# Performance work log

Measured on AMD Instinct MI355X. Metric: run time of the kernel, lower is better.

The kernel has to match this reference:

```python
import math
import jax, jax.numpy as jnp
import numpy as np
from jax import lax

MUL = 16           # multiplicity of 0e and 1o in input and output irreps
NRB = 8            # num_radial_basis
DIAMETER = 3.0
STEPS = (1.0, 1.0, 1.0)
DIM = 4 * MUL      # 16 scalars + 16 vectors * 3 = 64 channels


def _constants():
    # lattice from __init__: arange(-s, s+1) * step per axis, s = floor(r/step)
    r = DIAMETER / 2
    axes = [np.arange(-math.floor(r / st), math.floor(r / st) + 1.0) * st for st in STEPS]
    lattice = np.stack(np.meshgrid(*axes, indexing='ij'), axis=-1)  # [Kx,Ky,Kz,3]
    d = np.linalg.norm(lattice, axis=-1)                            # [Kx,Ky,Kz]
    # soft_one_hot_linspace(basis='smooth_finite', cutoff=True)
    values = np.linspace(0.0, r, NRB + 2)[1:-1]
    step = values[1] - values[0]
    diff = (d[..., None] - values) / step
    inside = diff ** 2 < 1.0
    emb = np.where(inside, 1.14136 * np.exp(2.0) * np.exp(-2.0 / np.where(inside, 1.0 - diff ** 2, 1.0)), 0.0)
    # spherical harmonics, normalize=True, normalization='component'
    n = lattice / np.maximum(d[..., None], 1e-12)  # unit vectors; 0 at the origin voxel
    sh0 = np.ones_like(d)                          # Y_0 (component normalized)
    sh1 = np.sqrt(3.0) * n                         # Y_1 (component normalized)
    return emb.astype(np.float32), sh0.astype(np.float32), sh1.astype(np.float32)

EMB, SH0, SH1 = _constants()
KX, KY, KZ = SH0.shape  # 3,3,3


def setup_inputs() -> dict:
    key = jax.random.key(0)
    ks = jax.random.split(key, 7)
    B, G = 4, 32
    return {
        'x': jax.random.normal(ks[0], (B, G, G, G, DIM), jnp.float32),
        'W_sc0': jax.random.normal(ks[1], (MUL, MUL), jnp.float32),  # Linear 0e->0e
        'W_sc1': jax.random.normal(ks[2], (MUL, MUL), jnp.float32),  # Linear 1o->1o
        'w1': jax.random.normal(ks[3], (NRB, MUL, MUL), jnp.float32),  # path 0e x 0e -> 0e
        'w2': jax.random.normal(ks[4], (NRB, MUL, MUL), jnp.float32),  # path 0e x 1o -> 1o
        'w3': jax.random.normal(ks[5], (NRB, MUL, MUL), jnp.float32),  # path 1o x 0e -> 1o
        'w4': jax.random.normal(ks[6], (NRB, MUL, MUL), jnp.float32),  # path 1o x 1o -> 0e
    }


def _kernel(w1, w2, w3, w4):
    # radial basis -> per-voxel path weights, divided by kernel volume (as in source)
    emb, sh0, sh1 = jnp.asarray(EMB), jnp.asarray(SH0), jnp.asarray(SH1)
    norm = float(KX * KY * KZ)
    W1, W2, W3, W4 = [jnp.einsum('xyzk,kio->xyzio', emb, w) / norm for w in (w1, w2, w3, w4)]
    # path normalization: each output irrep receives 2 paths of fan_in mul*1 = 16 -> 1/sqrt(32)
    alpha = 1.0 / np.sqrt(2.0 * MUL)
    # tp.right blocks (Clebsch-Gordan contractions, lmax=1):
    k00 = alpha * W1 * sh0[..., None, None]                                              # [.,i,o]
    k01 = alpha * jnp.einsum('xyzio,xyzm->xyziom', W2, sh1).reshape(KX, KY, KZ, MUL, 3 * MUL)
    k10 = (alpha / np.sqrt(3.0)) * jnp.einsum('xyzio,xyzm->xyzimo', W4, sh1).reshape(KX, KY, KZ, 3 * MUL, MUL)
    k11 = alpha * jnp.einsum('xyzio,mn->xyzimon', W3 * sh0[..., None, None],
                             jnp.eye(3, dtype=W3.dtype)).reshape(KX, KY, KZ, 3 * MUL, 3 * MUL)
    return jnp.concatenate([jnp.concatenate([k00, k01], axis=-1),
                            jnp.concatenate([k10, k11], axis=-1)], axis=-2)  # [Kx,Ky,Kz,64,64]


def reference(x, W_sc0, W_sc1, w1, w2, w3, w4):
    B, X, Y, Z, _ = x.shape
    inv_sqrt_mul = 1.0 / np.sqrt(MUL)
    # self-connection: e3nn Linear per irrep (applied pointwise over b,x,y,z)
    xs = x[..., :MUL]                                   # [B,X,Y,Z,16] scalars
    xv = x[..., MUL:].reshape(B, X, Y, Z, MUL, 3)       # [B,X,Y,Z,16,3] vectors
    sc_s = (xs @ W_sc0) * inv_sqrt_mul
    sc_v = jnp.einsum('bxyzic,io->bxyzoc', xv, W_sc1) * inv_sqrt_mul
    sc = jnp.concatenate([sc_s, sc_v.reshape(B, X, Y, Z, 3 * MUL)], axis=-1)
    # position-dependent equivariant kernel + standard 3D conv
    k = _kernel(w1, w2, w3, w4)
    conv = lax.conv_general_dilated(x, k, (1, 1, 1), 'SAME',
                                    dimension_numbers=('NXYZC', 'XYZIO', 'NXYZC'))
    return sc + conv
```

## Files before the change

### kernel.cpp

```cpp
#include <hip/hip_runtime.h>

typedef unsigned short u16;
typedef unsigned int u32;
typedef __bf16 bf16x8 __attribute__((ext_vector_type(8)));
typedef float f32x4 __attribute__((ext_vector_type(4)));
typedef u32 u32x4 __attribute__((ext_vector_type(4)));

__device__ __align__(16) u16 g_kTr[27 * 8 * 512];

__device__ __forceinline__ u16 f2bf(float f) {
    unsigned int u = __float_as_uint(f);
    u += 0x7FFFu + ((u >> 16) & 1u);
    return (u16)(u >> 16);
}

__device__ __forceinline__ u32 pack_bf(float a, float b) {
    u32 ua = __float_as_uint(a) + 0x8000u;
    u32 ub = __float_as_uint(b) + 0x8000u;
    return __builtin_amdgcn_perm(ub, ua, 0x07060302u);
}

__global__ __launch_bounds__(64) void build_k(
    const float* __restrict__ Wsc0, const float* __restrict__ Wsc1,
    const float* __restrict__ w1, const float* __restrict__ w2,
    const float* __restrict__ w3, const float* __restrict__ w4)
{
    const int t = blockIdx.x;
    const int c = threadIdx.x;
    const int dx = t / 9 - 1, dy = (t / 3) % 3 - 1, dz = t % 3 - 1;
    const float d = sqrtf((float)(dx * dx + dy * dy + dz * dz));
    const float step = 1.5f / 9.0f;
    float emb[8];
#pragma unroll
    for (int k = 0; k < 8; ++k) {
        float diff = (d - (float)(k + 1) * step) / step;
        float q = diff * diff;
        emb[k] = (q < 1.0f) ? 1.14136f * expf(2.0f - 2.0f / (1.0f - q)) : 0.0f;
    }
    const float dn = fmaxf(d, 1e-12f);
    const float s3 = 1.7320508075688772f;
    const float sh1[3] = { s3 * dx / dn, s3 * dy / dn, s3 * dz / dn };
    const float alpha  = 0.17677669529663687f;
    const float alpha3 = alpha * 0.57735026918962576f;

    const int base2 = ((t * 2 + (c >> 5)) * 2 + ((c >> 4) & 1)) * 2;
    const int l15c  = c & 15;
    auto put = [&](int r, float v) {
        g_kTr[(base2 + (r >> 5)) * 512 + (((r >> 3) & 3) * 16 + l15c) * 8 + (r & 7)] =
            f2bf(v);
    };

    if (c < 16) {
        const int o = c;
#pragma unroll
        for (int i = 0; i < 16; ++i) {
            float W1 = 0.f, W4 = 0.f;
#pragma unroll
            for (int k = 0; k < 8; ++k) {
                W1 += emb[k] * w1[k * 256 + i * 16 + o];
                W4 += emb[k] * w4[k * 256 + i * 16 + o];
            }
            W1 *= (1.0f / 27.0f); W4 *= (1.0f / 27.0f);
            float v0 = alpha * W1;
            if (t == 13) v0 += 0.25f * Wsc0[i * 16 + o];
            put(i, v0);
            const float base = alpha3 * W4;
#pragma unroll
            for (int m = 0; m < 3; ++m) put(16 + 3 * i + m, base * sh1[m]);
        }
    } else {
        const int o = (c - 16) / 3, nc = (c - 16) % 3;
#pragma unroll
        for (int i = 0; i < 16; ++i) {
            float W2 = 0.f, W3 = 0.f;
#pragma unroll
            for (int k = 0; k < 8; ++k) {
                W2 += emb[k] * w2[k * 256 + i * 16 + o];
                W3 += emb[k] * w3[k * 256 + i * 16 + o];
            }
            W2 *= (1.0f / 27.0f); W3 *= (1.0f / 27.0f);
            put(i, alpha * W2 * sh1[nc]);
#pragma unroll
            for (int m = 0; m < 3; ++m) {
                float v = (m == nc) ? alpha * W3 : 0.0f;
                if (t == 13 && m == nc) v += 0.25f * Wsc1[i * 16 + o];
                put(16 + 3 * i + m, v);
            }
        }
    }
}

#define LDSW7 24576

#define ISSUE_B(s, t) \
  { const char* _p = bTr + (t) * 8192; \
    asm volatile("global_load_dwordx4 %0, %4, off\n\t" \
                 "global_load_dwordx4 %1, %4, off offset:1024\n\t" \
                 "global_load_dwordx4 %2, %4, off offset:2048\n\t" \
                 "global_load_dwordx4 %3, %4, off offset:3072" \
                 : "=&v"(B##s##0), "=&v"(B##s##1), "=&v"(B##s##2), "=&v"(B##s##3) \
                 : "v"(_p)); }

#define LOADA2(s, i0, i1, RCC) { \
  const int _r  = rbase + (RCC); \
  const int _o0 = _r * 128 + ((kg ^ (_r & 7)) << 4); \
  A##s##_##i0 = *reinterpret_cast<const bf16x8*>(abase + _o0); \
  A##s##_##i1 = *reinterpret_cast<const bf16x8*>(abase + (_o0 ^ 64)); }

#define RCC7(T, YY) (((T)/9)*128 + ((((T)/3)%3) + (YY))*18 + ((T)%3))

#define LOAD_A4(s, T) \
  LOADA2(s, 0, 1, RCC7(T,0)) \
  LOADA2(s, 2, 3, RCC7(T,1))

#define WAITV(N) \
  asm volatile("s_waitcnt vmcnt(" #N ")" ::: "memory"); \
  __builtin_amdgcn_sched_barrier(0);

#define BC(x) __builtin_bit_cast(bf16x8, x)
#define MF(b_, a_, c_) __builtin_amdgcn_mfma_f32_16x16x32_bf16(BC(b_), a_, c_, 0, 0, 0)

#define MFMA8(bs, as) \
  acc00 = MF(B##bs##0, A##as##_0, acc00); acc01 = MF(B##bs##2, A##as##_0, acc01); \
  acc10 = MF(B##bs##0, A##as##_2, acc10); acc11 = MF(B##bs##2, A##as##_2, acc11); \
  acc00 = MF(B##bs##1, A##as##_1, acc00); acc01 = MF(B##bs##3, A##as##_1, acc01); \
  acc10 = MF(B##bs##1, A##as##_3, acc10); acc11 = MF(B##bs##3, A##as##_3, acc11);

__global__ __launch_bounds__(256, 3) void conv_mfma8(
    const float* __restrict__ x, float* __restrict__ out)
{
    __shared__ __align__(16) u16 xt[LDSW7];

    const int bid0 = blockIdx.x;
    const int bid  = (bid0 & 7) * 256 + (bid0 >> 3);
    const int b    = bid >> 9;
    const int X    = (bid >> 4) & 31;
    const int yg   = (bid >> 1) & 7;
    const int zg   = bid & 1;
    const int y0   = yg << 2;
    const int z0   = zg << 4;
    const int tid  = threadIdx.x;
    const int wv   = tid >> 6;
    const int lane = tid & 63;
    const int l15  = lane & 15;
    const int kg   = lane >> 4;
    const int yh   = wv >> 1;
    const int nh   = wv & 1;

    const char* bTr = (const char*)g_kTr + nh * 4096 + lane * 16;

    u32x4 B00, B01, B02, B03, B10, B11, B12, B13, B20, B21, B22, B23;
    bf16x8 A0_0, A0_1, A0_2, A0_3;
    bf16x8 A1_0, A1_1, A1_2, A1_3;

    ISSUE_B(0, 1)
    ISSUE_B(1, 3)

    {
        const int rloc = lane >> 3;
        const int swz  = (lane & 7) ^ rloc;
        const int cip  = wv * 4;
        const int rip0 = cip * 8 + rloc;
#pragma unroll 1
        for (int p = 0; p < 3; ++p) {
            const int xin = X + p - 1;
#pragma unroll
            for (int j = 0; j < 4; ++j) {
                const int rip = rip0 + j * 8;
                const int yi  = rip / 18;
                const int zid = rip - yi * 18;
                const int yin = y0 + yi - 1;
                const int zin = z0 + zid - 1;
                const bool inb = (rip < 108) & ((unsigned)xin < 32u)
                               & ((unsigned)yin < 32u) & ((unsigned)zin < 32u);
                u32x4 pk = {0u, 0u, 0u, 0u};
                if (inb) {
                    const float4* s = reinterpret_cast<const float4*>(
                        x + ((size_t)(((b * 32 + xin) * 32 + yin) * 32 + zin) * 64
                             + swz * 8));
                    float4 v0 = s[0], v1 = s[1];
                    pk[0] = pack_bf(v0.x, v0.y); pk[1] = pack_bf(v0.z, v0.w);
                    pk[2] = pack_bf(v1.x, v1.y); pk[3] = pack_bf(v1.z, v1.w);
                }
                *reinterpret_cast<u32x4*>(&xt[(p * 16 + cip + j) * 512 + lane * 8]) = pk;
            }
        }
    }
    __syncthreads();

    const char* abase = reinterpret_cast<const char*>(xt);
    const int rbase = yh * 36 + l15;

    const f32x4 z4 = {0.f, 0.f, 0.f, 0.f};
    f32x4 acc00 = z4, acc01 = z4, acc10 = z4, acc11 = z4;

    LOAD_A4(0, 1)
    ISSUE_B(2, 4)   LOAD_A4(1, 3)            MFMA8(0, 0)
    ISSUE_B(0, 5)   LOAD_A4(0, 4)            MFMA8(1, 1)
    ISSUE_B(1, 7)   LOAD_A4(1, 5)  WAITV(8)  MFMA8(2, 0)
    ISSUE_B(2, 9)   LOAD_A4(0, 7)  WAITV(8)  MFMA8(0, 1)
    ISSUE_B(0, 10)  LOAD_A4(1, 9)  WAITV(8)  MFMA8(1, 0)
    ISSUE_B(1, 11)  LOAD_A4(0, 10) WAITV(8)  MFMA8(2, 1)
    ISSUE_B(2, 12)  LOAD_A4(1, 11) WAITV(8)  MFMA8(0, 0)
    ISSUE_B(0, 13)  LOAD_A4(0, 12) WAITV(8)  MFMA8(1, 1)
    ISSUE_B(1, 14)  LOAD_A4(1, 13) WAITV(8)  MFMA8(2, 0)
    ISSUE_B(2, 15)  LOAD_A4(0, 14) WAITV(8)  MFMA8(0, 1)
    ISSUE_B(0, 16)  LOAD_A4(1, 15) WAITV(8)  MFMA8(1, 0)
    ISSUE_B(1, 17)  LOAD_A4(0, 16) WAITV(8)  MFMA8(2, 1)
    ISSUE_B(2, 19)  LOAD_A4(1, 17) WAITV(8)  MFMA8(0, 0)
    ISSUE_B(0, 21)  LOAD_A4(0, 19) WAITV(8)  MFMA8(1, 1)
    ISSUE_B(1, 22)  LOAD_A4(1, 21) WAITV(8)  MFMA8(2, 0)
    ISSUE_B(2, 23)  LOAD_A4(0, 22) WAITV(8)  MFMA8(0, 1)
    ISSUE_B(0, 25)  LOAD_A4(1, 23) WAITV(8)  MFMA8(1, 0)
                    LOAD_A4(0, 25) WAITV(4)  MFMA8(2, 1)
                                   WAITV(0)  MFMA8(0, 0)

    float* obase = out + ((((size_t)(b * 32 + X) * 32 + (y0 + yh * 2)) * 32) + z0) * 64
                 + nh * 32 + kg * 4;
    *reinterpret_cast<f32x4*>(obase + l15 * 64)               = acc00;
    *reinterpret_cast<f32x4*>(obase + l15 * 64 + 16)          = acc01;
    *reinterpret_cast<f32x4*>(obase + 2048 + l15 * 64)        = acc10;
    *reinterpret_cast<f32x4*>(obase + 2048 + l15 * 64 + 16)   = acc11;
}

extern "C" void kernel_launch(void* const* d_in, const int* in_sizes, int n_in,
                              void* d_out, int out_size, void* d_ws, size_t ws_size,
                              hipStream_t stream)
{
    const float* x    = (const float*)d_in[0];
    const float* Wsc0 = (const float*)d_in[1];
    const float* Wsc1 = (const float*)d_in[2];
    const float* w1   = (const float*)d_in[3];
    const float* w2   = (const float*)d_in[4];
    const float* w3   = (const float*)d_in[5];
    const float* w4   = (const float*)d_in[6];
    float* out = (float*)d_out;

    build_k<<<dim3(27), dim3(64), 0, stream>>>(Wsc0, Wsc1, w1, w2, w3, w4);
    conv_mfma8<<<dim3(2048), dim3(256), 0, stream>>>(x, out);
}
```

Before: 57.12 us.

## Pre-convert input to bf16 and use persistent double-buffered async-LDS conv kernel

Adds a prep pass that converts x to bf16 into workspace, merged into the same launch as the kernel-weight build. The new conv kernel runs 256 large-LDS blocks, each handling 4 tiles of 4 y-rows, with an 8-accumulator MFMA tile. It streams the next tile's halo into a second LDS buffer with global_load_lds while computing the current tile. This targets the fp32 conversion and load latency in the old conv, but costs an extra full pass over x and runs at low occupancy with a rigid hand-tuned wait schedule.

```diff
diff --git a/kernel.cpp b/kernel.cpp
--- a/kernel.cpp
+++ b/kernel.cpp
@@ -6,13 +6,10 @@
 typedef float f32x4 __attribute__((ext_vector_type(4)));
 typedef u32 u32x4 __attribute__((ext_vector_type(4)));
 
+#define AS1 __attribute__((address_space(1)))
+#define AS3 __attribute__((address_space(3)))
+
 __device__ __align__(16) u16 g_kTr[27 * 8 * 512];
-
-__device__ __forceinline__ u16 f2bf(float f) {
-    unsigned int u = __float_as_uint(f);
-    u += 0x7FFFu + ((u >> 16) & 1u);
-    return (u16)(u >> 16);
-}
 
 __device__ __forceinline__ u32 pack_bf(float a, float b) {
     u32 ua = __float_as_uint(a) + 0x8000u;
@@ -20,77 +17,95 @@
     return __builtin_amdgcn_perm(ub, ua, 0x07060302u);
 }
 
-__global__ __launch_bounds__(64) void build_k(
+__global__ __launch_bounds__(256) void prep(
     const float* __restrict__ Wsc0, const float* __restrict__ Wsc1,
     const float* __restrict__ w1, const float* __restrict__ w2,
-    const float* __restrict__ w3, const float* __restrict__ w4)
+    const float* __restrict__ w3, const float* __restrict__ w4,
+    const float* __restrict__ x, u16* __restrict__ xb, u32* __restrict__ zp)
 {
-    const int t = blockIdx.x;
-    const int c = threadIdx.x;
-    const int dx = t / 9 - 1, dy = (t / 3) % 3 - 1, dz = t % 3 - 1;
-    const float d = sqrtf((float)(dx * dx + dy * dy + dz * dz));
-    const float step = 1.5f / 9.0f;
-    float emb[8];
-#pragma unroll
-    for (int k = 0; k < 8; ++k) {
-        float diff = (d - (float)(k + 1) * step) / step;
-        float q = diff * diff;
-        emb[k] = (q < 1.0f) ? 1.14136f * expf(2.0f - 2.0f / (1.0f - q)) : 0.0f;
-    }
-    const float dn = fmaxf(d, 1e-12f);
-    const float s3 = 1.7320508075688772f;
-    const float sh1[3] = { s3 * dx / dn, s3 * dy / dn, s3 * dz / dn };
-    const float alpha  = 0.17677669529663687f;
-    const float alpha3 = alpha * 0.57735026918962576f;
-
-    const int base2 = ((t * 2 + (c >> 5)) * 2 + ((c >> 4) & 1)) * 2;
-    const int l15c  = c & 15;
-    auto put = [&](int r, float v) {
-        g_kTr[(base2 + (r >> 5)) * 512 + (((r >> 3) & 3) * 16 + l15c) * 8 + (r & 7)] =
-            f2bf(v);
-    };
-
-    if (c < 16) {
-        const int o = c;
-#pragma unroll
-        for (int i = 0; i < 16; ++i) {
-            float W1 = 0.f, W4 = 0.f;
-#pragma unroll
-            for (int k = 0; k < 8; ++k) {
-                W1 += emb[k] * w1[k * 256 + i * 16 + o];
-                W4 += emb[k] * w4[k * 256 + i * 16 + o];
+    const int tid = threadIdx.x;
+    if (blockIdx.x < 27) {
+        if (tid >= 64) return;
+        const int t = blockIdx.x;
+        const int c = tid;
+        const int dx = t / 9 - 1, dy = (t / 3) % 3 - 1, dz = t % 3 - 1;
+        const float d = sqrtf((float)(dx * dx + dy * dy + dz * dz));
+        const float step = 1.5f / 9.0f;
+        float emb[8];
+#pragma unroll
+        for (int k = 0; k < 8; ++k) {
+            float diff = (d - (float)(k + 1) * step) / step;
+            float q = diff * diff;
+            emb[k] = (q < 1.0f) ? 1.14136f * expf(2.0f - 2.0f / (1.0f - q)) : 0.0f;
+        }
+        const float dn = fmaxf(d, 1e-12f);
+        const float s3 = 1.7320508075688772f;
+        const float sh1[3] = { s3 * dx / dn, s3 * dy / dn, s3 * dz / dn };
+        const float alpha  = 0.17677669529663687f;
+        const float alpha3 = alpha * 0.57735026918962576f;
+
+        const int base2 = ((t * 2 + (c >> 5)) * 2 + ((c >> 4) & 1)) * 2;
+        const int l15c  = c & 15;
+        auto put = [&](int r, float v) {
+            u32 u = __float_as_uint(v);
+            u += 0x7FFFu + ((u >> 16) & 1u);
+            g_kTr[(base2 + (r >> 5)) * 512 + (((r >> 3) & 3) * 16 + l15c) * 8 + (r & 7)] =
+                (u16)(u >> 16);
+        };
+
+        if (c < 16) {
+            const int o = c;
+#pragma unroll
+            for (int i = 0; i < 16; ++i) {
+                float W1 = 0.f, W4 = 0.f;
+#pragma unroll
+                for (int k = 0; k < 8; ++k) {
+                    W1 += emb[k] * w1[k * 256 + i * 16 + o];
+                    W4 += emb[k] * w4[k * 256 + i * 16 + o];
+                }
+                W1 *= (1.0f / 27.0f); W4 *= (1.0f / 27.0f);
+                float v0 = alpha * W1;
+                if (t == 13) v0 += 0.25f * Wsc0[i * 16 + o];
+                put(i, v0);
+                const float base = alpha3 * W4;
+#pragma unroll
+                for (int m = 0; m < 3; ++m) put(16 + 3 * i + m, base * sh1[m]);
             }
-            W1 *= (1.0f / 27.0f); W4 *= (1.0f / 27.0f);
-            float v0 = alpha * W1;
-            if (t == 13) v0 += 0.25f * Wsc0[i * 16 + o];
-            put(i, v0);
-            const float base = alpha3 * W4;
-#pragma unroll
-            for (int m = 0; m < 3; ++m) put(16 + 3 * i + m, base * sh1[m]);
+        } else {
+            const int o = (c - 16) / 3, nc = (c - 16) % 3;
+#pragma unroll
+            for (int i = 0; i < 16; ++i) {
+                float W2 = 0.f, W3 = 0.f;
+#pragma unroll
+                for (int k = 0; k < 8; ++k) {
+                    W2 += emb[k] * w2[k * 256 + i * 16 + o];
+                    W3 += emb[k] * w3[k * 256 + i * 16 + o];
+                }
+                W2 *= (1.0f / 27.0f); W3 *= (1.0f / 27.0f);
+                put(i, alpha * W2 * sh1[nc]);
+#pragma unroll
+                for (int m = 0; m < 3; ++m) {
+                    float v = (m == nc) ? alpha * W3 : 0.0f;
+                    if (t == 13 && m == nc) v += 0.25f * Wsc1[i * 16 + o];
+                    put(16 + 3 * i + m, v);
+                }
+            }
         }
     } else {
-        const int o = (c - 16) / 3, nc = (c - 16) % 3;
-#pragma unroll
-        for (int i = 0; i < 16; ++i) {
-            float W2 = 0.f, W3 = 0.f;
-#pragma unroll
-            for (int k = 0; k < 8; ++k) {
-                W2 += emb[k] * w2[k * 256 + i * 16 + o];
-                W3 += emb[k] * w3[k * 256 + i * 16 + o];
-            }
-            W2 *= (1.0f / 27.0f); W3 *= (1.0f / 27.0f);
-            put(i, alpha * W2 * sh1[nc]);
-#pragma unroll
-            for (int m = 0; m < 3; ++m) {
-                float v = (m == nc) ? alpha * W3 : 0.0f;
-                if (t == 13 && m == nc) v += 0.25f * Wsc1[i * 16 + o];
-                put(16 + 3 * i + m, v);
-            }
+        const int bid2 = blockIdx.x - 27;
+        if (bid2 == 0) {
+            u32x4 z = {0u, 0u, 0u, 0u};
+            *reinterpret_cast<u32x4*>(zp + tid * 4) = z;
         }
+        const size_t base = ((size_t)bid2 * 256 + tid) * 8;
+        const float4* s = reinterpret_cast<const float4*>(x + base);
+        float4 v0 = s[0], v1 = s[1];
+        u32x4 p;
+        p[0] = pack_bf(v0.x, v0.y); p[1] = pack_bf(v0.z, v0.w);
+        p[2] = pack_bf(v1.x, v1.y); p[3] = pack_bf(v1.z, v1.w);
+        *reinterpret_cast<u32x4*>(xb + base) = p;
     }
 }
-
-#define LDSW7 24576
 
 #define ISSUE_B(s, t) \
   { const char* _p = bTr + (t) * 8192; \
@@ -107,18 +122,159 @@
   A##s##_##i0 = *reinterpret_cast<const bf16x8*>(abase + _o0); \
   A##s##_##i1 = *reinterpret_cast<const bf16x8*>(abase + (_o0 ^ 64)); }
 
+#define WAITV(N) \
+  asm volatile("s_waitcnt vmcnt(" #N ")" ::: "memory"); \
+  __builtin_amdgcn_sched_barrier(0);
+
+#define BARRIER() \
+  asm volatile("s_waitcnt lgkmcnt(0)\n\ts_barrier" ::: "memory"); \
+  __builtin_amdgcn_sched_barrier(0);
+
+#define BC(x) __builtin_bit_cast(bf16x8, x)
+#define MF(b_, a_, c_) __builtin_amdgcn_mfma_f32_16x16x32_bf16(BC(b_), a_, c_, 0, 0, 0)
+
+#define BUFU16 39424
+
+#define STG(s) { \
+  const int _c   = wv * 20 + (s); \
+  const int _row = _c * 8 + rloc; \
+  const int _rid = _row / 204; \
+  const int _rem = _row - _rid * 204; \
+  const int _yi  = _rem / 34; \
+  const int _zid = _rem - _yi * 34; \
+  const int _xin = Xs + _rid - 1; \
+  const int _yin = ys0 + _yi - 1; \
+  const int _zin = _zid - 1; \
+  const bool _ib = (_row < 612) && ((unsigned)_xin < 32u) \
+                 && ((unsigned)_yin < 32u) && ((unsigned)_zin < 32u); \
+  const u16* _src = _ib \
+      ? xb + ((size_t)(((bs * 32 + _xin) * 32 + _yin) * 32 + _zin) * 64 + swz * 8) \
+      : zp16; \
+  u16* _dst = (_c < 77) ? (bufn + _c * 512) : (xt + 78848); \
+  __builtin_amdgcn_global_load_lds((const AS1 u32*)_src, (AS3 u32*)_dst, 16, 0, 0); \
+  __builtin_amdgcn_sched_barrier(0); }
+
+#define RCC4(T, YY, MT) ((((T)/9)*6 + (YY) + (((T)/3)%3))*34 + ((T)%3) + (MT)*16)
+
+#define LOAD_A8(s, T) \
+  LOADA2(s, 0, 1, RCC4(T,0,0)) \
+  LOADA2(s, 2, 3, RCC4(T,0,1)) \
+  LOADA2(s, 4, 5, RCC4(T,1,0)) \
+  LOADA2(s, 6, 7, RCC4(T,1,1))
+
+#define MFMA16(bs, as) \
+  acc000 = MF(B##bs##0, A##as##_0, acc000); acc001 = MF(B##bs##2, A##as##_0, acc001); \
+  acc010 = MF(B##bs##0, A##as##_2, acc010); acc011 = MF(B##bs##2, A##as##_2, acc011); \
+  acc100 = MF(B##bs##0, A##as##_4, acc100); acc101 = MF(B##bs##2, A##as##_4, acc101); \
+  acc110 = MF(B##bs##0, A##as##_6, acc110); acc111 = MF(B##bs##2, A##as##_6, acc111); \
+  acc000 = MF(B##bs##1, A##as##_1, acc000); acc001 = MF(B##bs##3, A##as##_1, acc001); \
+  acc010 = MF(B##bs##1, A##as##_3, acc010); acc011 = MF(B##bs##3, A##as##_3, acc011); \
+  acc100 = MF(B##bs##1, A##as##_5, acc100); acc101 = MF(B##bs##3, A##as##_5, acc101); \
+  acc110 = MF(B##bs##1, A##as##_7, acc110); acc111 = MF(B##bs##3, A##as##_7, acc111);
+
+__global__ __launch_bounds__(256, 1) void conv_mfma10(
+    const u16* __restrict__ xb, const u16* __restrict__ zp16,
+    float* __restrict__ out)
+{
+    extern __shared__ u16 xt[];
+
+    const int blk   = blockIdx.x;
+    const int tbase = ((blk & 7) * 32 + (blk >> 3)) * 4;
+    const int tid   = threadIdx.x;
+    const int wv    = tid >> 6;
+    const int lane  = tid & 63;
+    const int l15   = lane & 15;
+    const int kg    = lane >> 4;
+    const int yh    = wv >> 1;
+    const int nh    = wv & 1;
+    const int rloc  = lane >> 3;
+    const int swz   = (lane & 7) ^ rloc;
+    const int rbase = yh * 68 + l15;
+
+    const char* bTr = (const char*)g_kTr + nh * 4096 + lane * 16;
+
+    u32x4 B00, B01, B02, B03, B10, B11, B12, B13,
+          B20, B21, B22, B23, B30, B31, B32, B33;
+    bf16x8 A0_0, A0_1, A0_2, A0_3, A0_4, A0_5, A0_6, A0_7;
+    bf16x8 A1_0, A1_1, A1_2, A1_3, A1_4, A1_5, A1_6, A1_7;
+
+    {
+        const int ts = tbase;
+        const int bs = ts >> 8, Xs = (ts >> 3) & 31, ys0 = (ts & 7) << 2;
+        u16* bufn = xt;
+        STG(0)  STG(1)  STG(2)  STG(3)  STG(4)
+        STG(5)  STG(6)  STG(7)  STG(8)  STG(9)
+        STG(10) STG(11) STG(12) STG(13) STG(14)
+        STG(15) STG(16) STG(17) STG(18) STG(19)
+        WAITV(0)
+    }
+    ISSUE_B(0, 1)
+    ISSUE_B(1, 3)
+    ISSUE_B(2, 4)
+    BARRIER()
+
+#pragma unroll 1
+    for (int k = 0; k < 4; ++k) {
+        const u16* bufk = xt + (k & 1) * BUFU16;
+        u16*       bufn = xt + ((k & 1) ^ 1) * BUFU16;
+        const char* abase = (const char*)bufk;
+
+        const int tk = tbase + k;
+        const int b  = tk >> 8, X = (tk >> 3) & 31, y0 = (tk & 7) << 2;
+        const int ts = tbase + (k < 3 ? k + 1 : 3);
+        const int bs = ts >> 8, Xs = (ts >> 3) & 31, ys0 = (ts & 7) << 2;
+
+        const f32x4 z4 = {0.f, 0.f, 0.f, 0.f};
+        f32x4 acc000 = z4, acc001 = z4, acc010 = z4, acc011 = z4;
+        f32x4 acc100 = z4, acc101 = z4, acc110 = z4, acc111 = z4;
+
+        LOAD_A8(0, 1)
+        STG(0)  STG(1)  ISSUE_B(3, 5)   LOAD_A8(1, 3)   WAITV(14)  MFMA16(0, 0)
+        STG(2)  STG(3)  ISSUE_B(0, 7)   LOAD_A8(0, 4)   WAITV(16)  MFMA16(1, 1)
+        STG(4)  STG(5)  ISSUE_B(1, 9)   LOAD_A8(1, 5)   WAITV(18)  MFMA16(2, 0)
+        STG(6)  STG(7)  ISSUE_B(2, 10)  LOAD_A8(0, 7)   WAITV(18)  MFMA16(3, 1)
+        STG(8)  STG(9)  ISSUE_B(3, 11)  LOAD_A8(1, 9)   WAITV(18)  MFMA16(0, 0)
+        STG(10) STG(11) ISSUE_B(0, 12)  LOAD_A8(0, 10)  WAITV(18)  MFMA16(1, 1)
+        STG(12) STG(13) ISSUE_B(1, 13)  LOAD_A8(1, 11)  WAITV(18)  MFMA16(2, 0)
+        STG(14) STG(15) ISSUE_B(2, 14)  LOAD_A8(0, 12)  WAITV(18)  MFMA16(3, 1)
+        STG(16) STG(17) ISSUE_B(3, 15)  LOAD_A8(1, 13)  WAITV(18)  MFMA16(0, 0)
+        STG(18) STG(19) ISSUE_B(0, 16)  LOAD_A8(0, 14)  WAITV(18)  MFMA16(1, 1)
+                        ISSUE_B(1, 17)  LOAD_A8(1, 15)  WAITV(16)  MFMA16(2, 0)
+                        ISSUE_B(2, 19)  LOAD_A8(0, 16)  WAITV(14)  MFMA16(3, 1)
+                        ISSUE_B(3, 21)  LOAD_A8(1, 17)  WAITV(12)  MFMA16(0, 0)
+                        ISSUE_B(0, 22)  LOAD_A8(0, 19)  WAITV(12)  MFMA16(1, 1)
+                        ISSUE_B(1, 23)  LOAD_A8(1, 21)  WAITV(12)  MFMA16(2, 0)
+                        ISSUE_B(2, 25)  LOAD_A8(0, 22)  WAITV(12)  MFMA16(3, 1)
+                                        LOAD_A8(1, 23)  WAITV(8)   MFMA16(0, 0)
+                                        LOAD_A8(0, 25)  WAITV(4)   MFMA16(1, 1)
+                                                        WAITV(0)   MFMA16(2, 0)
+
+        float* obase = out + (((size_t)(b * 32 + X) * 32 + (y0 + yh * 2)) * 32) * 64
+                     + nh * 32 + kg * 4;
+        *reinterpret_cast<f32x4*>(obase + l15 * 64)                    = acc000;
+        *reinterpret_cast<f32x4*>(obase + l15 * 64 + 16)               = acc001;
+        *reinterpret_cast<f32x4*>(obase + (16 + l15) * 64)             = acc010;
+        *reinterpret_cast<f32x4*>(obase + (16 + l15) * 64 + 16)        = acc011;
+        *reinterpret_cast<f32x4*>(obase + 2048 + l15 * 64)             = acc100;
+        *reinterpret_cast<f32x4*>(obase + 2048 + l15 * 64 + 16)        = acc101;
+        *reinterpret_cast<f32x4*>(obase + 2048 + (16 + l15) * 64)      = acc110;
+        *reinterpret_cast<f32x4*>(obase + 2048 + (16 + l15) * 64 + 16) = acc111;
+        __builtin_amdgcn_sched_barrier(0);
+
+        ISSUE_B(0, 1)
+        ISSUE_B(1, 3)
+        ISSUE_B(2, 4)
+        BARRIER()
+    }
+}
+
+#define LDSW7 24576
+
 #define RCC7(T, YY) (((T)/9)*128 + ((((T)/3)%3) + (YY))*18 + ((T)%3))
 
 #define LOAD_A4(s, T) \
   LOADA2(s, 0, 1, RCC7(T,0)) \
   LOADA2(s, 2, 3, RCC7(T,1))
-
-#define WAITV(N) \
-  asm volatile("s_waitcnt vmcnt(" #N ")" ::: "memory"); \
-  __builtin_amdgcn_sched_barrier(0);
-
-#define BC(x) __builtin_bit_cast(bf16x8, x)
-#define MF(b_, a_, c_) __builtin_amdgcn_mfma_f32_16x16x32_bf16(BC(b_), a_, c_, 0, 0, 0)
 
 #define MFMA8(bs, as) \
   acc00 = MF(B##bs##0, A##as##_0, acc00); acc01 = MF(B##bs##2, A##as##_0, acc01); \
@@ -236,6 +392,16 @@
     const float* w4   = (const float*)d_in[6];
     float* out = (float*)d_out;
 
-    build_k<<<dim3(27), dim3(64), 0, stream>>>(Wsc0, Wsc1, w1, w2, w3, w4);
-    conv_mfma8<<<dim3(2048), dim3(256), 0, stream>>>(x, out);
+    const size_t xb_bytes = (size_t)4 * 32 * 32 * 32 * 64 * 2;
+    if (ws_size >= 4096 + xb_bytes) {
+        u32* zp = (u32*)d_ws;
+        u16* xb = (u16*)((char*)d_ws + 4096);
+        prep<<<dim3(27 + 4096), dim3(256), 0, stream>>>(Wsc0, Wsc1, w1, w2, w3, w4,
+                                                        x, xb, zp);
+        conv_mfma10<<<dim3(256), dim3(256), 158720, stream>>>(xb, (const u16*)zp, out);
+    } else {
+        prep<<<dim3(27), dim3(256), 0, stream>>>(Wsc0, Wsc1, w1, w2, w3, w4,
+                                                 x, (u16*)nullptr, (u32*)nullptr);
+        conv_mfma8<<<dim3(2048), dim3(256), 0, stream>>>(x, out);
+    }
 }
```

Measured after the change: 55.19 us. 1.03x faster.

## Use persistent blocks with double-buffered LDS staging of next tile

Applied to the files above, without the earlier changes.

Replaces the 2048-block conv kernel with 256 persistent blocks that each process four consecutive full-Z tiles of 4 y-rows. The halo for the next tile is loaded from global memory and packed into a second LDS buffer while MFMAs run on the current one, which hides staging latency behind compute. Each wave now owns twice as many output rows (8 accumulators), and B loads switch from inline asm with explicit vmcnt waits to plain loads ordered by sched barriers. The cost is roughly 154KB of dynamic LDS and one block per CU, so occupancy-based latency hiding is gone and the kernel depends on the compiler scheduling the interleaved loads well.

```diff
diff --git a/kernel.cpp b/kernel.cpp
--- a/kernel.cpp
+++ b/kernel.cpp
@@ -7,12 +7,6 @@
 typedef u32 u32x4 __attribute__((ext_vector_type(4)));
 
 __device__ __align__(16) u16 g_kTr[27 * 8 * 512];
-
-__device__ __forceinline__ u16 f2bf(float f) {
-    unsigned int u = __float_as_uint(f);
-    u += 0x7FFFu + ((u >> 16) & 1u);
-    return (u16)(u >> 16);
-}
 
 __device__ __forceinline__ u32 pack_bf(float a, float b) {
     u32 ua = __float_as_uint(a) + 0x8000u;
@@ -46,8 +40,10 @@
     const int base2 = ((t * 2 + (c >> 5)) * 2 + ((c >> 4) & 1)) * 2;
     const int l15c  = c & 15;
     auto put = [&](int r, float v) {
+        u32 u = __float_as_uint(v);
+        u += 0x7FFFu + ((u >> 16) & 1u);
         g_kTr[(base2 + (r >> 5)) * 512 + (((r >> 3) & 3) * 16 + l15c) * 8 + (r & 7)] =
-            f2bf(v);
+            (u16)(u >> 16);
     };
 
     if (c < 16) {
@@ -90,16 +86,13 @@
     }
 }
 
-#define LDSW7 24576
-
-#define ISSUE_B(s, t) \
-  { const char* _p = bTr + (t) * 8192; \
-    asm volatile("global_load_dwordx4 %0, %4, off\n\t" \
-                 "global_load_dwordx4 %1, %4, off offset:1024\n\t" \
-                 "global_load_dwordx4 %2, %4, off offset:2048\n\t" \
-                 "global_load_dwordx4 %3, %4, off offset:3072" \
-                 : "=&v"(B##s##0), "=&v"(B##s##1), "=&v"(B##s##2), "=&v"(B##s##3) \
-                 : "v"(_p)); }
+#define BUFU16 39424
+
+#define WALL() __builtin_amdgcn_sched_barrier(0);
+
+#define LOADB(S, T) { \
+  const u32x4* _p = reinterpret_cast<const u32x4*>(bTr + (T) * 8192); \
+  B##S##0 = _p[0]; B##S##1 = _p[64]; B##S##2 = _p[128]; B##S##3 = _p[192]; }
 
 #define LOADA2(s, i0, i1, RCC) { \
   const int _r  = rbase + (RCC); \
@@ -107,120 +100,145 @@
   A##s##_##i0 = *reinterpret_cast<const bf16x8*>(abase + _o0); \
   A##s##_##i1 = *reinterpret_cast<const bf16x8*>(abase + (_o0 ^ 64)); }
 
-#define RCC7(T, YY) (((T)/9)*128 + ((((T)/3)%3) + (YY))*18 + ((T)%3))
-
-#define LOAD_A4(s, T) \
-  LOADA2(s, 0, 1, RCC7(T,0)) \
-  LOADA2(s, 2, 3, RCC7(T,1))
-
-#define WAITV(N) \
-  asm volatile("s_waitcnt vmcnt(" #N ")" ::: "memory"); \
-  __builtin_amdgcn_sched_barrier(0);
+#define RCC4(T, YY, MT) ((((T)/9)*6 + (YY) + (((T)/3)%3))*34 + ((T)%3) + (MT)*16)
+
+#define LOAD_A8(s, T) \
+  LOADA2(s, 0, 1, RCC4(T,0,0)) \
+  LOADA2(s, 2, 3, RCC4(T,0,1)) \
+  LOADA2(s, 4, 5, RCC4(T,1,0)) \
+  LOADA2(s, 6, 7, RCC4(T,1,1))
+
+#define SLD(S, C) { \
+  const int _c   = wv * 20 + (C); \
+  const int _row = _c * 8 + rloc; \
+  const int _rid = _row / 204; \
+  const int _rem = _row - _rid * 204; \
+  const int _yi  = _rem / 34; \
+  const int _zid = _rem - _yi * 34; \
+  const int _xin = Xs + _rid - 1; \
+  const int _yin = ys0 + _yi - 1; \
+  const int _zin = _zid - 1; \
+  const bool _ib = (_row < 612) && ((unsigned)_xin < 32u) && \
+                   ((unsigned)_yin < 32u) && ((unsigned)_zin < 32u); \
+  F##S##a = (f32x4){0.f, 0.f, 0.f, 0.f}; \
+  F##S##b = (f32x4){0.f, 0.f, 0.f, 0.f}; \
+  if (_ib) { \
+    const f32x4* _p = reinterpret_cast<const f32x4*>( \
+        x + ((size_t)(((bs * 32 + _xin) * 32 + _yin) * 32 + _zin) * 64 + swz * 8)); \
+    F##S##a = _p[0]; F##S##b = _p[1]; \
+  } }
+
+#define SWR(S, C) { \
+  const int _c = wv * 20 + (C); \
+  if (_c < 77) { \
+    u32x4 _pk; \
+    _pk[0] = pack_bf(F##S##a[0], F##S##a[1]); \
+    _pk[1] = pack_bf(F##S##a[2], F##S##a[3]); \
+    _pk[2] = pack_bf(F##S##b[0], F##S##b[1]); \
+    _pk[3] = pack_bf(F##S##b[2], F##S##b[3]); \
+    *reinterpret_cast<u32x4*>(bufn + _c * 512 + lane * 8) = _pk; \
+  } }
 
 #define BC(x) __builtin_bit_cast(bf16x8, x)
 #define MF(b_, a_, c_) __builtin_amdgcn_mfma_f32_16x16x32_bf16(BC(b_), a_, c_, 0, 0, 0)
 
-#define MFMA8(bs, as) \
-  acc00 = MF(B##bs##0, A##as##_0, acc00); acc01 = MF(B##bs##2, A##as##_0, acc01); \
-  acc10 = MF(B##bs##0, A##as##_2, acc10); acc11 = MF(B##bs##2, A##as##_2, acc11); \
-  acc00 = MF(B##bs##1, A##as##_1, acc00); acc01 = MF(B##bs##3, A##as##_1, acc01); \
-  acc10 = MF(B##bs##1, A##as##_3, acc10); acc11 = MF(B##bs##3, A##as##_3, acc11);
-
-__global__ __launch_bounds__(256, 3) void conv_mfma8(
+#define MFMA16(bs, as) \
+  acc000 = MF(B##bs##0, A##as##_0, acc000); acc001 = MF(B##bs##2, A##as##_0, acc001); \
+  acc010 = MF(B##bs##0, A##as##_2, acc010); acc011 = MF(B##bs##2, A##as##_2, acc011); \
+  acc100 = MF(B##bs##0, A##as##_4, acc100); acc101 = MF(B##bs##2, A##as##_4, acc101); \
+  acc110 = MF(B##bs##0, A##as##_6, acc110); acc111 = MF(B##bs##2, A##as##_6, acc111); \
+  acc000 = MF(B##bs##1, A##as##_1, acc000); acc001 = MF(B##bs##3, A##as##_1, acc001); \
+  acc010 = MF(B##bs##1, A##as##_3, acc010); acc011 = MF(B##bs##3, A##as##_3, acc011); \
+  acc100 = MF(B##bs##1, A##as##_5, acc100); acc101 = MF(B##bs##3, A##as##_5, acc101); \
+  acc110 = MF(B##bs##1, A##as##_7, acc110); acc111 = MF(B##bs##3, A##as##_7, acc111);
+
+__global__ __launch_bounds__(256, 1) void conv_mfma11(
     const float* __restrict__ x, float* __restrict__ out)
 {
-    __shared__ __align__(16) u16 xt[LDSW7];
-
-    const int bid0 = blockIdx.x;
-    const int bid  = (bid0 & 7) * 256 + (bid0 >> 3);
-    const int b    = bid >> 9;
-    const int X    = (bid >> 4) & 31;
-    const int yg   = (bid >> 1) & 7;
-    const int zg   = bid & 1;
-    const int y0   = yg << 2;
-    const int z0   = zg << 4;
-    const int tid  = threadIdx.x;
-    const int wv   = tid >> 6;
-    const int lane = tid & 63;
-    const int l15  = lane & 15;
-    const int kg   = lane >> 4;
-    const int yh   = wv >> 1;
-    const int nh   = wv & 1;
+    extern __shared__ u16 xt[];
+
+    const int blk   = blockIdx.x;
+    const int tbase = ((blk & 7) * 32 + (blk >> 3)) * 4;
+    const int tid   = threadIdx.x;
+    const int wv    = tid >> 6;
+    const int lane  = tid & 63;
+    const int l15   = lane & 15;
+    const int kg    = lane >> 4;
+    const int yh    = wv >> 1;
+    const int nh    = wv & 1;
+    const int rloc  = lane >> 3;
+    const int swz   = (lane & 7) ^ rloc;
+    const int rbase = yh * 68 + l15;
 
     const char* bTr = (const char*)g_kTr + nh * 4096 + lane * 16;
 
     u32x4 B00, B01, B02, B03, B10, B11, B12, B13, B20, B21, B22, B23;
-    bf16x8 A0_0, A0_1, A0_2, A0_3;
-    bf16x8 A1_0, A1_1, A1_2, A1_3;
-
-    ISSUE_B(0, 1)
-    ISSUE_B(1, 3)
+    bf16x8 A0_0, A0_1, A0_2, A0_3, A0_4, A0_5, A0_6, A0_7;
+    bf16x8 A1_0, A1_1, A1_2, A1_3, A1_4, A1_5, A1_6, A1_7;
+    f32x4 F0a, F0b, F1a, F1b, F2a, F2b, F3a, F3b;
 
     {
-        const int rloc = lane >> 3;
-        const int swz  = (lane & 7) ^ rloc;
-        const int cip  = wv * 4;
-        const int rip0 = cip * 8 + rloc;
+        const int ts = tbase;
+        const int bs = ts >> 8, Xs = (ts >> 3) & 31, ys0 = (ts & 7) << 2;
+        u16* bufn = xt;
+#pragma unroll
+        for (int g = 0; g < 5; ++g) {
+            SLD(0, g * 4 + 0) SLD(1, g * 4 + 1) SLD(2, g * 4 + 2) SLD(3, g * 4 + 3)
+            SWR(0, g * 4 + 0) SWR(1, g * 4 + 1) SWR(2, g * 4 + 2) SWR(3, g * 4 + 3)
+        }
+    }
+    __syncthreads();
+
 #pragma unroll 1
-        for (int p = 0; p < 3; ++p) {
-            const int xin = X + p - 1;
-#pragma unroll
-            for (int j = 0; j < 4; ++j) {
-                const int rip = rip0 + j * 8;
-                const int yi  = rip / 18;
-                const int zid = rip - yi * 18;
-                const int yin = y0 + yi - 1;
-                const int zin = z0 + zid - 1;
-                const bool inb = (rip < 108) & ((unsigned)xin < 32u)
-                               & ((unsigned)yin < 32u) & ((unsigned)zin < 32u);
-                u32x4 pk = {0u, 0u, 0u, 0u};
-                if (inb) {
-                    const float4* s = reinterpret_cast<const float4*>(
-                        x + ((size_t)(((b * 32 + xin) * 32 + yin) * 32 + zin) * 64
-                             + swz * 8));
-                    float4 v0 = s[0], v1 = s[1];
-                    pk[0] = pack_bf(v0.x, v0.y); pk[1] = pack_bf(v0.z, v0.w);
-                    pk[2] = pack_bf(v1.x, v1.y); pk[3] = pack_bf(v1.z, v1.w);
-                }
-                *reinterpret_cast<u32x4*>(&xt[(p * 16 + cip + j) * 512 + lane * 8]) = pk;
-            }
-        }
-    }
-    __syncthreads();
-
-    const char* abase = reinterpret_cast<const char*>(xt);
-    const int rbase = yh * 36 + l15;
-
-    const f32x4 z4 = {0.f, 0.f, 0.f, 0.f};
-    f32x4 acc00 = z4, acc01 = z4, acc10 = z4, acc11 = z4;
-
-    LOAD_A4(0, 1)
-    ISSUE_B(2, 4)   LOAD_A4(1, 3)            MFMA8(0, 0)
-    ISSUE_B(0, 5)   LOAD_A4(0, 4)            MFMA8(1, 1)
-    ISSUE_B(1, 7)   LOAD_A4(1, 5)  WAITV(8)  MFMA8(2, 0)
-    ISSUE_B(2, 9)   LOAD_A4(0, 7)  WAITV(8)  MFMA8(0, 1)
-    ISSUE_B(0, 10)  LOAD_A4(1, 9)  WAITV(8)  MFMA8(1, 0)
-    ISSUE_B(1, 11)  LOAD_A4(0, 10) WAITV(8)  MFMA8(2, 1)
-    ISSUE_B(2, 12)  LOAD_A4(1, 11) WAITV(8)  MFMA8(0, 0)
-    ISSUE_B(0, 13)  LOAD_A4(0, 12) WAITV(8)  MFMA8(1, 1)
-    ISSUE_B(1, 14)  LOAD_A4(1, 13) WAITV(8)  MFMA8(2, 0)
-    ISSUE_B(2, 15)  LOAD_A4(0, 14) WAITV(8)  MFMA8(0, 1)
-    ISSUE_B(0, 16)  LOAD_A4(1, 15) WAITV(8)  MFMA8(1, 0)
-    ISSUE_B(1, 17)  LOAD_A4(0, 16) WAITV(8)  MFMA8(2, 1)
-    ISSUE_B(2, 19)  LOAD_A4(1, 17) WAITV(8)  MFMA8(0, 0)
-    ISSUE_B(0, 21)  LOAD_A4(0, 19) WAITV(8)  MFMA8(1, 1)
-    ISSUE_B(1, 22)  LOAD_A4(1, 21) WAITV(8)  MFMA8(2, 0)
-    ISSUE_B(2, 23)  LOAD_A4(0, 22) WAITV(8)  MFMA8(0, 1)
-    ISSUE_B(0, 25)  LOAD_A4(1, 23) WAITV(8)  MFMA8(1, 0)
-                    LOAD_A4(0, 25) WAITV(4)  MFMA8(2, 1)
-                                   WAITV(0)  MFMA8(0, 0)
-
-    float* obase = out + ((((size_t)(b * 32 + X) * 32 + (y0 + yh * 2)) * 32) + z0) * 64
-                 + nh * 32 + kg * 4;
-    *reinterpret_cast<f32x4*>(obase + l15 * 64)               = acc00;
-    *reinterpret_cast<f32x4*>(obase + l15 * 64 + 16)          = acc01;
-    *reinterpret_cast<f32x4*>(obase + 2048 + l15 * 64)        = acc10;
-    *reinterpret_cast<f32x4*>(obase + 2048 + l15 * 64 + 16)   = acc11;
+    for (int k = 0; k < 4; ++k) {
+        const u16* bufk = xt + (k & 1) * BUFU16;
+        u16*       bufn = xt + ((k & 1) ^ 1) * BUFU16;
+        const char* abase = (const char*)bufk;
+
+        const int tk = tbase + k;
+        const int b  = tk >> 8, X = (tk >> 3) & 31, y0 = (tk & 7) << 2;
+        const int ts = tbase + (k < 3 ? k + 1 : 3);
+        const int bs = ts >> 8, Xs = (ts >> 3) & 31, ys0 = (ts & 7) << 2;
+
+        const f32x4 z4 = {0.f, 0.f, 0.f, 0.f};
+        f32x4 acc000 = z4, acc001 = z4, acc010 = z4, acc011 = z4;
+        f32x4 acc100 = z4, acc101 = z4, acc110 = z4, acc111 = z4;
+
+        LOADB(0, 1) LOADB(1, 3) LOAD_A8(0, 1)
+        WALL()
+        SLD(0,0)  SLD(1,1)              LOADB(2, 4)  LOAD_A8(1, 3)  MFMA16(0, 0) WALL()
+        SLD(2,2)  SLD(3,3)              LOADB(0, 5)  LOAD_A8(0, 4)  MFMA16(1, 1) WALL()
+        SWR(0,0)  SWR(1,1)  SLD(0,4)  SLD(1,5)   LOADB(1, 7)  LOAD_A8(1, 5)  MFMA16(2, 0) WALL()
+        SWR(2,2)  SWR(3,3)  SLD(2,6)  SLD(3,7)   LOADB(2, 9)  LOAD_A8(0, 7)  MFMA16(0, 1) WALL()
+        SWR(0,4)  SWR(1,5)  SLD(0,8)  SLD(1,9)   LOADB(0, 10) LOAD_A8(1, 9)  MFMA16(1, 0) WALL()
+        SWR(2,6)  SWR(3,7)  SLD(2,10) SLD(3,11)  LOADB(1, 11) LOAD_A8(0, 10) MFMA16(2, 1) WALL()
+        SWR(0,8)  SWR(1,9)  SLD(0,12) SLD(1,13)  LOADB(2, 12) LOAD_A8(1, 11) MFMA16(0, 0) WALL()
+        SWR(2,10) SWR(3,11) SLD(2,14) SLD(3,15)  LOADB(0, 13) LOAD_A8(0, 12) MFMA16(1, 1) WALL()
+        SWR(0,12) SWR(1,13) SLD(0,16) SLD(1,17)  LOADB(1, 14) LOAD_A8(1, 13) MFMA16(2, 0) WALL()
+        SWR(2,14) SWR(3,15) SLD(2,18) SLD(3,19)  LOADB(2, 15) LOAD_A8(0, 14) MFMA16(0, 1) WALL()
+        SWR(0,16) SWR(1,17)                      LOADB(0, 16) LOAD_A8(1, 15) MFMA16(1, 0) WALL()
+        SWR(2,18) SWR(3,19)                      LOADB(1, 17) LOAD_A8(0, 16) MFMA16(2, 1) WALL()
+                                                 LOADB(2, 19) LOAD_A8(1, 17) MFMA16(0, 0) WALL()
+                                                 LOADB(0, 21) LOAD_A8(0, 19) MFMA16(1, 1) WALL()
+                                                 LOADB(1, 22) LOAD_A8(1, 21) MFMA16(2, 0) WALL()
+                                                 LOADB(2, 23) LOAD_A8(0, 22) MFMA16(0, 1) WALL()
+                                                 LOADB(0, 25) LOAD_A8(1, 23) MFMA16(1, 0) WALL()
+                                                              LOAD_A8(0, 25) MFMA16(2, 1) WALL()
+                                                                             MFMA16(0, 0) WALL()
+
+        float* obase = out + (((size_t)(b * 32 + X) * 32 + (y0 + yh * 2)) * 32) * 64
+                     + nh * 32 + kg * 4;
+        *reinterpret_cast<f32x4*>(obase + l15 * 64)                    = acc000;
+        *reinterpret_cast<f32x4*>(obase + l15 * 64 + 16)               = acc001;
+        *reinterpret_cast<f32x4*>(obase + (16 + l15) * 64)             = acc010;
+        *reinterpret_cast<f32x4*>(obase + (16 + l15) * 64 + 16)        = acc011;
+        *reinterpret_cast<f32x4*>(obase + 2048 + l15 * 64)             = acc100;
+        *reinterpret_cast<f32x4*>(obase + 2048 + l15 * 64 + 16)        = acc101;
+        *reinterpret_cast<f32x4*>(obase + 2048 + (16 + l15) * 64)      = acc110;
+        *reinterpret_cast<f32x4*>(obase + 2048 + (16 + l15) * 64 + 16) = acc111;
+
+        __syncthreads();
+    }
 }
 
 extern "C" void kernel_launch(void* const* d_in, const int* in_sizes, int n_in,
@@ -237,5 +255,5 @@
     float* out = (float*)d_out;
 
     build_k<<<dim3(27), dim3(64), 0, stream>>>(Wsc0, Wsc1, w1, w2, w3, w4);
-    conv_mfma8<<<dim3(2048), dim3(256), 0, stream>>>(x, out);
-}
+    conv_mfma11<<<dim3(256), dim3(256), 2 * 78848, stream>>>(x, out);
+}
```

Result: faster. 54.59 us (-4.4%).
